# Kernel tuning notes

Measured on AMD Instinct MI355X. Metric: run time of the kernel, lower is better.

## Reference

```python
import jax, jax.numpy as jnp
import numpy as np

D = 1024
H = 16
HD = D // H
FF = 4 * D
LN_EPS = 1e-5


def _layernorm(x, g, b):
    mu = jnp.mean(x, axis=-1, keepdims=True)
    var = jnp.mean(jnp.square(x - mu), axis=-1, keepdims=True)
    return (x - mu) / jnp.sqrt(var + LN_EPS) * g + b


def setup_inputs() -> dict:
    key = jax.random.key(0)
    ks = jax.random.split(key, 17)
    s = 0.02
    inp = {
        "x": jax.random.normal(ks[0], (2, 2048, D), dtype=jnp.float32),
        "Wq": jax.random.normal(ks[1], (D, D), dtype=jnp.float32) * s,
        "bq": jnp.zeros((D,), jnp.float32),
        "Wk": jax.random.normal(ks[2], (D, D), dtype=jnp.float32) * s,
        "bk": jnp.zeros((D,), jnp.float32),
        "Wv": jax.random.normal(ks[3], (D, D), dtype=jnp.float32) * s,
        "bv": jnp.zeros((D,), jnp.float32),
        "Wo": jax.random.normal(ks[4], (D, D), dtype=jnp.float32) * s,
        "bo": jnp.zeros((D,), jnp.float32),
        "ln1_g": jnp.ones((D,), jnp.float32),
        "ln1_b": jnp.zeros((D,), jnp.float32),
        "W1": jax.random.normal(ks[5], (D, FF), dtype=jnp.float32) * s,
        "b1": jnp.zeros((FF,), jnp.float32),
        "W2": jax.random.normal(ks[6], (FF, D), dtype=jnp.float32) * s,
        "b2": jnp.zeros((D,), jnp.float32),
        "ln2_g": jnp.ones((D,), jnp.float32),
        "ln2_b": jnp.zeros((D,), jnp.float32),
    }
    return inp


def reference(x, Wq, bq, Wk, bk, Wv, bv, Wo, bo, ln1_g, ln1_b, W1, b1, W2, b2, ln2_g, ln2_b):
    bs, seq, _ = x.shape
    # qkv projections -> [b, h, s, hd]
    def split_heads(t):
        return t.reshape(bs, seq, H, HD).transpose(0, 2, 1, 3)
    q = split_heads(x @ Wq + bq)
    k = split_heads(x @ Wk + bk)
    v = split_heads(x @ Wv + bv)
    # causal attention (explicit, matching source math)
    scores = jnp.einsum('bhqd,bhkd->bhqk', q, k) / jnp.sqrt(jnp.float32(HD))
    causal = jnp.tril(jnp.ones((seq, seq), dtype=bool))
    scores = jnp.where(causal, scores, -jnp.inf)
    attn = jax.nn.softmax(scores, axis=-1)
    ctx = jnp.einsum('bhqk,bhkd->bhqd', attn, v)
    ctx = ctx.transpose(0, 2, 1, 3).reshape(bs, seq, D)
    attn_out = ctx @ Wo + bo
    # residual + LN1
    h = _layernorm(attn_out + x, ln1_g, ln1_b)
    # GELU MLP (exact erf gelu, torch nn.GELU default)
    ffn = jax.nn.gelu(h @ W1 + b1, approximate=False) @ W2 + b2
    # residual + LN2
    out = _layernorm(ffn + h, ln2_g, ln2_b)
    return out
```

## Files before the change

### kernel.cpp

```cpp
#include <hip/hip_runtime.h>

#define D_MODEL 1024
#define SEQ 2048
#define NHEAD 16
#define HDIM 64
#define FF_DIM 4096
#define NTOK 4096

using bf16x8 = __attribute__((ext_vector_type(8))) short;
using f32x4  = __attribute__((ext_vector_type(4))) float;
typedef unsigned short ushort_t;

__device__ __forceinline__ unsigned short f2bu(float f) {
    unsigned int u = __float_as_uint(f);
    unsigned int r = u + 0x7FFFu + ((u >> 16) & 1u);
    return (unsigned short)(r >> 16);
}
__device__ __forceinline__ float b2f(unsigned short u) {
    union { unsigned int i; float f; } x;
    x.i = ((unsigned int)u) << 16;
    return x.f;
}

typedef __attribute__((address_space(1))) const unsigned int* gas_ptr;
typedef __attribute__((address_space(3))) unsigned int* las_ptr;
__device__ __forceinline__ void gload_lds16(const void* g, void* l) {
    __builtin_amdgcn_global_load_lds((gas_ptr)g, (las_ptr)l, 16, 0, 0);
}

__device__ __forceinline__ float gelu_f(float x) {
    float z = 1.59576912f * x * (1.f + 0.044715f * x * x);
    float t = __expf(z);
    float th = (t - 1.f) / (t + 1.f);
    return 0.5f * x * (1.f + th);
}

__global__ void cast_f32_to_bf16(const float* __restrict__ in, ushort_t* __restrict__ out, int n8) {
    int i = blockIdx.x * blockDim.x + threadIdx.x;
    if (i >= n8) return;
    const float4* p = (const float4*)in + (size_t)i * 2;
    float4 a = p[0], b = p[1];
    uint4 o;
    o.x = (unsigned)f2bu(a.x) | ((unsigned)f2bu(a.y) << 16);
    o.y = (unsigned)f2bu(a.z) | ((unsigned)f2bu(a.w) << 16);
    o.z = (unsigned)f2bu(b.x) | ((unsigned)f2bu(b.y) << 16);
    o.w = (unsigned)f2bu(b.z) | ((unsigned)f2bu(b.w) << 16);
    ((uint4*)out)[i] = o;
}

__global__ void transpose_f32_to_bf16(const float* __restrict__ in, ushort_t* __restrict__ out, int R, int C) {
    __shared__ float tile[64][65];
    int bx = blockIdx.x * 64, by = blockIdx.y * 64;
    int tx = threadIdx.x & 63, ty = threadIdx.x >> 6;
#pragma unroll
    for (int i = 0; i < 64; i += 4)
        tile[ty + i][tx] = in[(size_t)(by + ty + i) * C + bx + tx];
    __syncthreads();
#pragma unroll
    for (int i = 0; i < 64; i += 4)
        out[(size_t)(bx + ty + i) * R + by + tx] = f2bu(tile[tx][ty + i]);
}

__global__ __launch_bounds__(256)
void gemm_bf16(const ushort_t* __restrict__ A, const ushort_t* __restrict__ Bt,
               const float* __restrict__ bias, int bias_per_row,
               ushort_t* __restrict__ outb, float* __restrict__ outf,
               int M, int N, int K, float out_scale, int do_gelu) {
    __shared__ char lds[2 * 128 * 128];
    char* Al = lds;
    char* Bl = lds + 128 * 128;
    const int tid = threadIdx.x;
    const int l = tid & 63, w = tid >> 6;
    const int wr = w >> 1, wc = w & 1;
    const int g = l >> 4, l15 = l & 15;
    const int m0 = blockIdx.x * 128, n0 = blockIdx.y * 128;

    f32x4 acc[4][4] = {};
    const int nk = K >> 6;
    const int srow = l >> 3;
    const int scol = (l & 7) * 8;
    const ushort_t* Ab = A + (size_t)(m0 + w * 32 + srow) * K + scol;
    const ushort_t* Bb = Bt + (size_t)(n0 + w * 32 + srow) * K + scol;

    for (int kt = 0; kt < nk; ++kt) {
        __syncthreads();
        const size_t ko = (size_t)kt * 64;
#pragma unroll
        for (int c = 0; c < 4; ++c) {
            gload_lds16(Ab + (size_t)c * 8 * K + ko, Al + (w * 4 + c) * 1024);
            gload_lds16(Bb + (size_t)c * 8 * K + ko, Bl + (w * 4 + c) * 1024);
        }
        __syncthreads();
#pragma unroll
        for (int ks = 0; ks < 2; ks++) {
            bf16x8 af[4];
#pragma unroll
            for (int m = 0; m < 4; m++)
                af[m] = *(const bf16x8*)(Al + (wr * 64 + m * 16 + l15) * 128 + (ks * 4 + g) * 16);
#pragma unroll
            for (int n = 0; n < 4; n++) {
                bf16x8 bfr = *(const bf16x8*)(Bl + (wc * 64 + n * 16 + l15) * 128 + (ks * 4 + g) * 16);
#pragma unroll
                for (int m = 0; m < 4; m++)
                    acc[m][n] = __builtin_amdgcn_mfma_f32_16x16x32_bf16(af[m], bfr, acc[m][n], 0, 0, 0);
            }
        }
    }
#pragma unroll
    for (int m = 0; m < 4; m++) {
        int row0 = m0 + wr * 64 + m * 16 + g * 4;
#pragma unroll
        for (int n = 0; n < 4; n++) {
            int col = n0 + wc * 64 + n * 16 + l15;
            float bc = bias_per_row ? 0.f : bias[col];
#pragma unroll
            for (int jj = 0; jj < 4; jj++) {
                int row = row0 + jj;
                float v = acc[m][n][jj] + (bias_per_row ? bias[row] : bc);
                v *= out_scale;
                if (do_gelu) v = gelu_f(v);
                size_t idx = (size_t)row * N + col;
                if (outb) outb[idx] = f2bu(v);
                else      outf[idx] = v;
            }
        }
    }
}

__global__ __launch_bounds__(256)
void attn_fwd(const ushort_t* __restrict__ qg, const ushort_t* __restrict__ kg,
              const ushort_t* __restrict__ vtg, ushort_t* __restrict__ ctx) {
    __shared__ char plds[4 * 16 * 144];
    const int tid = threadIdx.x;
    const int l = tid & 63, w = tid >> 6;
    const int g = l >> 4, l15 = l & 15;
    const int bid = blockIdx.x;
    const int xcd = bid & 7;
    const int slot = bid >> 3;
    const int QBi = slot & 31;
    const int grp = slot >> 5;
    const int h = xcd + 8 * (grp & 1);
    const int b = grp >> 1;
    const int q0 = QBi * 64;
    const int qrow = b * SEQ + q0 + w * 16 + l15;
    const int q_local = w * 16 + l15;

    const ushort_t* qp = qg + (size_t)qrow * D_MODEL + h * HDIM + g * 8;
    bf16x8 qf0 = *(const bf16x8*)qp;
    bf16x8 qf1 = *(const bf16x8*)(qp + 32);

    const ushort_t* kbase = kg + ((size_t)(b * SEQ + l15) * D_MODEL) + h * HDIM + g * 8;
    const ushort_t* vbase = vtg + (size_t)(h * HDIM + l15) * NTOK + b * SEQ + g * 8;

    f32x4 O[4] = {};
    float m_run = -1e30f, l_run = 0.f;
    char* pl = plds + w * (16 * 144) + l15 * 144;

    bf16x8 kf[8];
    bf16x8 vf[8];
#pragma unroll
    for (int md = 0; md < 4; ++md) {
        const ushort_t* kp = kbase + (size_t)(md * 16) * D_MODEL;
        kf[2 * md]     = *(const bf16x8*)kp;
        kf[2 * md + 1] = *(const bf16x8*)(kp + 32);
    }

    for (int t = 0; t <= QBi; ++t) {
        const int kv0 = t * 64;
#pragma unroll
        for (int md = 0; md < 4; ++md) {
            const ushort_t* vp = vbase + (size_t)(md * 16) * NTOK + kv0;
            vf[2 * md]     = *(const bf16x8*)vp;
            vf[2 * md + 1] = *(const bf16x8*)(vp + 32);
        }
        f32x4 s[4];
#pragma unroll
        for (int md = 0; md < 4; ++md) {
            f32x4 z = {0.f, 0.f, 0.f, 0.f};
            z = __builtin_amdgcn_mfma_f32_16x16x32_bf16(kf[2 * md], qf0, z, 0, 0, 0);
            z = __builtin_amdgcn_mfma_f32_16x16x32_bf16(kf[2 * md + 1], qf1, z, 0, 0, 0);
            s[md] = z;
        }
        {
            const int tn = (t < QBi) ? (t + 1) : t;
#pragma unroll
            for (int md = 0; md < 4; ++md) {
                const ushort_t* kp = kbase + (size_t)(tn * 64 + md * 16) * D_MODEL;
                kf[2 * md]     = *(const bf16x8*)kp;
                kf[2 * md + 1] = *(const bf16x8*)(kp + 32);
            }
        }
        if (t == QBi) {
#pragma unroll
            for (int md = 0; md < 4; ++md)
#pragma unroll
                for (int jj = 0; jj < 4; jj++) {
                    int kvl = md * 16 + g * 4 + jj;
                    if (kvl > q_local) s[md][jj] = -1e30f;
                }
        }
        float pmax = -1e30f;
#pragma unroll
        for (int md = 0; md < 4; ++md)
#pragma unroll
            for (int jj = 0; jj < 4; jj++) pmax = fmaxf(pmax, s[md][jj]);
        pmax = fmaxf(pmax, __shfl_xor(pmax, 16));
        pmax = fmaxf(pmax, __shfl_xor(pmax, 32));
        float mnew = fmaxf(m_run, pmax);
        float sc = __expf(m_run - mnew);
        float rsum = 0.f;
#pragma unroll
        for (int md = 0; md < 4; ++md) {
            float p0 = __expf(s[md][0] - mnew);
            float p1 = __expf(s[md][1] - mnew);
            float p2 = __expf(s[md][2] - mnew);
            float p3 = __expf(s[md][3] - mnew);
            rsum += (p0 + p1) + (p2 + p3);
            uint2 pk;
            pk.x = (unsigned)f2bu(p0) | ((unsigned)f2bu(p1) << 16);
            pk.y = (unsigned)f2bu(p2) | ((unsigned)f2bu(p3) << 16);
            *(uint2*)(pl + (md * 16 + g * 4) * 2) = pk;
        }
        rsum += __shfl_xor(rsum, 16);
        rsum += __shfl_xor(rsum, 32);
        l_run = l_run * sc + rsum;
        m_run = mnew;
#pragma unroll
        for (int md = 0; md < 4; ++md) {
            O[md][0] *= sc; O[md][1] *= sc; O[md][2] *= sc; O[md][3] *= sc;
        }
#pragma unroll
        for (int ks = 0; ks < 2; ++ks) {
            bf16x8 pf = *(const bf16x8*)(pl + ks * 64 + g * 16);
#pragma unroll
            for (int md = 0; md < 4; ++md)
                O[md] = __builtin_amdgcn_mfma_f32_16x16x32_bf16(vf[2 * md + ks], pf, O[md], 0, 0, 0);
        }
    }
    float rl = 1.f / l_run;
#pragma unroll
    for (int md = 0; md < 4; ++md) {
        uint2 o;
        o.x = (unsigned)f2bu(O[md][0] * rl) | ((unsigned)f2bu(O[md][1] * rl) << 16);
        o.y = (unsigned)f2bu(O[md][2] * rl) | ((unsigned)f2bu(O[md][3] * rl) << 16);
        *(uint2*)(ctx + (size_t)qrow * D_MODEL + h * HDIM + md * 16 + g * 4) = o;
    }
}

__global__ __launch_bounds__(256)
void ln_kernel(const ushort_t* __restrict__ a, const ushort_t* __restrict__ resb,
               const float* __restrict__ resf,
               const float* __restrict__ gam, const float* __restrict__ bet,
               ushort_t* __restrict__ outb, float* __restrict__ outf) {
    const int w = threadIdx.x >> 6, l = threadIdx.x & 63;
    const int row = blockIdx.x * 4 + w;
    const size_t base = (size_t)row * D_MODEL + l * 16;
    float r[16];
    int4 av0 = *(const int4*)(a + base);
    int4 av1 = *(const int4*)(a + base + 8);
    const unsigned short* u0 = (const unsigned short*)&av0;
    const unsigned short* u1 = (const unsigned short*)&av1;
#pragma unroll
    for (int i = 0; i < 8; i++) { r[i] = b2f(u0[i]); r[8 + i] = b2f(u1[i]); }
    if (resf) {
        const float4* rp = (const float4*)(resf + base);
#pragma unroll
        for (int i = 0; i < 4; i++) {
            float4 f = rp[i];
            r[i * 4 + 0] += f.x; r[i * 4 + 1] += f.y; r[i * 4 + 2] += f.z; r[i * 4 + 3] += f.w;
        }
    } else {
        int4 rv0 = *(const int4*)(resb + base);
        int4 rv1 = *(const int4*)(resb + base + 8);
        const unsigned short* v0 = (const unsigned short*)&rv0;
        const unsigned short* v1 = (const unsigned short*)&rv1;
#pragma unroll
        for (int i = 0; i < 8; i++) { r[i] += b2f(v0[i]); r[8 + i] += b2f(v1[i]); }
    }
    float s = 0.f;
#pragma unroll
    for (int i = 0; i < 16; i++) s += r[i];
#pragma unroll
    for (int m = 1; m < 64; m <<= 1) s += __shfl_xor(s, m);
    float mu = s * (1.f / 1024.f);
    float v = 0.f;
#pragma unroll
    for (int i = 0; i < 16; i++) { float d = r[i] - mu; v += d * d; }
#pragma unroll
    for (int m = 1; m < 64; m <<= 1) v += __shfl_xor(v, m);
    float rstd = rsqrtf(v * (1.f / 1024.f) + 1e-5f);
    float o[16];
    const float4* gp = (const float4*)(gam + l * 16);
    const float4* bp = (const float4*)(bet + l * 16);
#pragma unroll
    for (int i = 0; i < 4; i++) {
        float4 gv = gp[i], bv = bp[i];
        o[i * 4 + 0] = (r[i * 4 + 0] - mu) * rstd * gv.x + bv.x;
        o[i * 4 + 1] = (r[i * 4 + 1] - mu) * rstd * gv.y + bv.y;
        o[i * 4 + 2] = (r[i * 4 + 2] - mu) * rstd * gv.z + bv.z;
        o[i * 4 + 3] = (r[i * 4 + 3] - mu) * rstd * gv.w + bv.w;
    }
    if (outb) {
        uint4 w0, w1;
        unsigned* pw0 = (unsigned*)&w0;
        unsigned* pw1 = (unsigned*)&w1;
#pragma unroll
        for (int i = 0; i < 4; i++) {
            pw0[i] = (unsigned)f2bu(o[i * 2]) | ((unsigned)f2bu(o[i * 2 + 1]) << 16);
            pw1[i] = (unsigned)f2bu(o[8 + i * 2]) | ((unsigned)f2bu(o[8 + i * 2 + 1]) << 16);
        }
        *(uint4*)(outb + base) = w0;
        *(uint4*)(outb + base + 8) = w1;
    } else {
        float4* op = (float4*)(outf + base);
#pragma unroll
        for (int i = 0; i < 4; i++)
            op[i] = make_float4(o[i * 4], o[i * 4 + 1], o[i * 4 + 2], o[i * 4 + 3]);
    }
}

extern "C" void kernel_launch(void* const* d_in, const int* in_sizes, int n_in,
                              void* d_out, int out_size, void* d_ws, size_t ws_size,
                              hipStream_t stream) {
    const float* x     = (const float*)d_in[0];
    const float* Wq    = (const float*)d_in[1];
    const float* bq    = (const float*)d_in[2];
    const float* Wk    = (const float*)d_in[3];
    const float* bk    = (const float*)d_in[4];
    const float* Wv    = (const float*)d_in[5];
    const float* bv    = (const float*)d_in[6];
    const float* Wo    = (const float*)d_in[7];
    const float* bo    = (const float*)d_in[8];
    const float* ln1_g = (const float*)d_in[9];
    const float* ln1_b = (const float*)d_in[10];
    const float* W1    = (const float*)d_in[11];
    const float* b1    = (const float*)d_in[12];
    const float* W2    = (const float*)d_in[13];
    const float* b2    = (const float*)d_in[14];
    const float* ln2_g = (const float*)d_in[15];
    const float* ln2_b = (const float*)d_in[16];
    float* out = (float*)d_out;

    char* ws = (char*)d_ws;
    const size_t SZ = (size_t)NTOK * D_MODEL * 2;
    ushort_t* xb  = (ushort_t*)(ws + 0 * SZ);
    ushort_t* qb  = (ushort_t*)(ws + 1 * SZ);
    ushort_t* kb  = (ushort_t*)(ws + 2 * SZ);
    ushort_t* vt  = (ushort_t*)(ws + 3 * SZ);
    ushort_t* ctx = (ushort_t*)(ws + 4 * SZ);
    ushort_t* aob = (ushort_t*)(ws + 5 * SZ);
    ushort_t* hb  = (ushort_t*)(ws + 6 * SZ);
    char* wts = ws + 7 * SZ;
    ushort_t* wqt = (ushort_t*)(wts + 0x000000);
    ushort_t* wkt = (ushort_t*)(wts + 0x200000);
    ushort_t* wvt = (ushort_t*)(wts + 0x400000);
    ushort_t* wot = (ushort_t*)(wts + 0x600000);
    ushort_t* w1t = (ushort_t*)(wts + 0x800000);
    ushort_t* w2t = (ushort_t*)(wts + 0x1000000);
    ushort_t* f1b = (ushort_t*)(ws + 0 * SZ);
    ushort_t* f2b = (ushort_t*)(ws + 4 * SZ);
    if (ws_size < (size_t)(7 * SZ) + 0x1800000) return;

    cast_f32_to_bf16<<<2048, 256, 0, stream>>>(x, xb, NTOK * D_MODEL / 8);
    transpose_f32_to_bf16<<<dim3(16, 16), 256, 0, stream>>>(Wq, wqt, 1024, 1024);
    transpose_f32_to_bf16<<<dim3(16, 16), 256, 0, stream>>>(Wk, wkt, 1024, 1024);
    transpose_f32_to_bf16<<<dim3(16, 16), 256, 0, stream>>>(Wv, wvt, 1024, 1024);
    transpose_f32_to_bf16<<<dim3(16, 16), 256, 0, stream>>>(Wo, wot, 1024, 1024);
    transpose_f32_to_bf16<<<dim3(64, 16), 256, 0, stream>>>(W1, w1t, 1024, 4096);
    transpose_f32_to_bf16<<<dim3(16, 64), 256, 0, stream>>>(W2, w2t, 4096, 1024);

    gemm_bf16<<<dim3(32, 8), 256, 0, stream>>>(xb, wqt, bq, 0, qb, nullptr, 4096, 1024, 1024, 0.125f, 0);
    gemm_bf16<<<dim3(32, 8), 256, 0, stream>>>(xb, wkt, bk, 0, kb, nullptr, 4096, 1024, 1024, 1.f, 0);
    gemm_bf16<<<dim3(8, 32), 256, 0, stream>>>(wvt, xb, bv, 1, vt, nullptr, 1024, 4096, 1024, 1.f, 0);

    attn_fwd<<<1024, 256, 0, stream>>>(qb, kb, vt, ctx);

    gemm_bf16<<<dim3(32, 8), 256, 0, stream>>>(ctx, wot, bo, 0, aob, nullptr, 4096, 1024, 1024, 1.f, 0);
    ln_kernel<<<1024, 256, 0, stream>>>(aob, nullptr, x, ln1_g, ln1_b, hb, nullptr);
    gemm_bf16<<<dim3(32, 32), 256, 0, stream>>>(hb, w1t, b1, 0, f1b, nullptr, 4096, 4096, 1024, 1.f, 1);
    gemm_bf16<<<dim3(32, 8), 256, 0, stream>>>(f1b, w2t, b2, 0, f2b, nullptr, 4096, 1024, 4096, 1.f, 0);
    ln_kernel<<<1024, 256, 0, stream>>>(f2b, hb, nullptr, ln2_g, ln2_b, nullptr, out);
}
```

Before: 593.0 us.

## Pair causal query blocks per attention CTA and use narrower GEMM tiles for N=1024

Each attention block now handles two query tiles, p and 31-p, so every CTA does roughly equal causal work, and the grid is halved to 512. The GEMM becomes a template on tile width BN, and the N=1024 projections and W2 use 128x64 tiles to double the CTA count and fill more CUs. Smaller tiles lower data reuse per CTA and add extra loads of the A operand, and the paired attention runs its two tiles one after the other within a block.

```diff
diff --git a/kernel.cpp b/kernel.cpp
--- a/kernel.cpp
+++ b/kernel.cpp
@@ -61,35 +61,39 @@
         out[(size_t)(bx + ty + i) * R + by + tx] = f2bu(tile[tx][ty + i]);
 }
 
+template<int BN>
 __global__ __launch_bounds__(256)
 void gemm_bf16(const ushort_t* __restrict__ A, const ushort_t* __restrict__ Bt,
                const float* __restrict__ bias, int bias_per_row,
                ushort_t* __restrict__ outb, float* __restrict__ outf,
                int M, int N, int K, float out_scale, int do_gelu) {
-    __shared__ char lds[2 * 128 * 128];
+    constexpr int NB  = BN / 32;
+    constexpr int BCH = BN / 32;
+    __shared__ char lds[(128 + BN) * 128];
     char* Al = lds;
     char* Bl = lds + 128 * 128;
     const int tid = threadIdx.x;
     const int l = tid & 63, w = tid >> 6;
     const int wr = w >> 1, wc = w & 1;
     const int g = l >> 4, l15 = l & 15;
-    const int m0 = blockIdx.x * 128, n0 = blockIdx.y * 128;
-
-    f32x4 acc[4][4] = {};
+    const int m0 = blockIdx.x * 128, n0 = blockIdx.y * BN;
+
+    f32x4 acc[4][NB] = {};
     const int nk = K >> 6;
     const int srow = l >> 3;
     const int scol = (l & 7) * 8;
     const ushort_t* Ab = A + (size_t)(m0 + w * 32 + srow) * K + scol;
-    const ushort_t* Bb = Bt + (size_t)(n0 + w * 32 + srow) * K + scol;
+    const ushort_t* Bb = Bt + (size_t)(n0 + w * (BN / 4) + srow) * K + scol;
 
     for (int kt = 0; kt < nk; ++kt) {
         __syncthreads();
         const size_t ko = (size_t)kt * 64;
 #pragma unroll
-        for (int c = 0; c < 4; ++c) {
+        for (int c = 0; c < 4; ++c)
             gload_lds16(Ab + (size_t)c * 8 * K + ko, Al + (w * 4 + c) * 1024);
-            gload_lds16(Bb + (size_t)c * 8 * K + ko, Bl + (w * 4 + c) * 1024);
-        }
+#pragma unroll
+        for (int c = 0; c < BCH; ++c)
+            gload_lds16(Bb + (size_t)c * 8 * K + ko, Bl + (w * BCH + c) * 1024);
         __syncthreads();
 #pragma unroll
         for (int ks = 0; ks < 2; ks++) {
@@ -98,8 +102,8 @@
             for (int m = 0; m < 4; m++)
                 af[m] = *(const bf16x8*)(Al + (wr * 64 + m * 16 + l15) * 128 + (ks * 4 + g) * 16);
 #pragma unroll
-            for (int n = 0; n < 4; n++) {
-                bf16x8 bfr = *(const bf16x8*)(Bl + (wc * 64 + n * 16 + l15) * 128 + (ks * 4 + g) * 16);
+            for (int n = 0; n < NB; n++) {
+                bf16x8 bfr = *(const bf16x8*)(Bl + (wc * (BN / 2) + n * 16 + l15) * 128 + (ks * 4 + g) * 16);
 #pragma unroll
                 for (int m = 0; m < 4; m++)
                     acc[m][n] = __builtin_amdgcn_mfma_f32_16x16x32_bf16(af[m], bfr, acc[m][n], 0, 0, 0);
@@ -110,8 +114,8 @@
     for (int m = 0; m < 4; m++) {
         int row0 = m0 + wr * 64 + m * 16 + g * 4;
 #pragma unroll
-        for (int n = 0; n < 4; n++) {
-            int col = n0 + wc * 64 + n * 16 + l15;
+        for (int n = 0; n < NB; n++) {
+            int col = n0 + wc * (BN / 2) + n * 16 + l15;
             float bc = bias_per_row ? 0.f : bias[col];
 #pragma unroll
             for (int jj = 0; jj < 4; jj++) {
@@ -137,113 +141,118 @@
     const int bid = blockIdx.x;
     const int xcd = bid & 7;
     const int slot = bid >> 3;
-    const int QBi = slot & 31;
-    const int grp = slot >> 5;
+    const int p = slot & 15;
+    const int grp = slot >> 4;
     const int h = xcd + 8 * (grp & 1);
     const int b = grp >> 1;
-    const int q0 = QBi * 64;
-    const int qrow = b * SEQ + q0 + w * 16 + l15;
     const int q_local = w * 16 + l15;
-
-    const ushort_t* qp = qg + (size_t)qrow * D_MODEL + h * HDIM + g * 8;
-    bf16x8 qf0 = *(const bf16x8*)qp;
-    bf16x8 qf1 = *(const bf16x8*)(qp + 32);
 
     const ushort_t* kbase = kg + ((size_t)(b * SEQ + l15) * D_MODEL) + h * HDIM + g * 8;
     const ushort_t* vbase = vtg + (size_t)(h * HDIM + l15) * NTOK + b * SEQ + g * 8;
-
-    f32x4 O[4] = {};
-    float m_run = -1e30f, l_run = 0.f;
     char* pl = plds + w * (16 * 144) + l15 * 144;
 
     bf16x8 kf[8];
     bf16x8 vf[8];
-#pragma unroll
-    for (int md = 0; md < 4; ++md) {
-        const ushort_t* kp = kbase + (size_t)(md * 16) * D_MODEL;
-        kf[2 * md]     = *(const bf16x8*)kp;
-        kf[2 * md + 1] = *(const bf16x8*)(kp + 32);
-    }
-
-    for (int t = 0; t <= QBi; ++t) {
-        const int kv0 = t * 64;
+
+#pragma unroll
+    for (int phase = 0; phase < 2; ++phase) {
+        const int QBi = phase ? (31 - p) : p;
+        const int qrow = b * SEQ + QBi * 64 + w * 16 + l15;
+
+        const ushort_t* qp = qg + (size_t)qrow * D_MODEL + h * HDIM + g * 8;
+        bf16x8 qf0 = *(const bf16x8*)qp;
+        bf16x8 qf1 = *(const bf16x8*)(qp + 32);
+
+        f32x4 O[4] = {};
+        float m_run = -1e30f, l_run = 0.f;
+
 #pragma unroll
         for (int md = 0; md < 4; ++md) {
-            const ushort_t* vp = vbase + (size_t)(md * 16) * NTOK + kv0;
-            vf[2 * md]     = *(const bf16x8*)vp;
-            vf[2 * md + 1] = *(const bf16x8*)(vp + 32);
-        }
-        f32x4 s[4];
+            const ushort_t* kp = kbase + (size_t)(md * 16) * D_MODEL;
+            kf[2 * md]     = *(const bf16x8*)kp;
+            kf[2 * md + 1] = *(const bf16x8*)(kp + 32);
+        }
+
+        for (int t = 0; t <= QBi; ++t) {
+            const int kv0 = t * 64;
+#pragma unroll
+            for (int md = 0; md < 4; ++md) {
+                const ushort_t* vp = vbase + (size_t)(md * 16) * NTOK + kv0;
+                vf[2 * md]     = *(const bf16x8*)vp;
+                vf[2 * md + 1] = *(const bf16x8*)(vp + 32);
+            }
+            f32x4 s[4];
+#pragma unroll
+            for (int md = 0; md < 4; ++md) {
+                f32x4 z = {0.f, 0.f, 0.f, 0.f};
+                z = __builtin_amdgcn_mfma_f32_16x16x32_bf16(kf[2 * md], qf0, z, 0, 0, 0);
+                z = __builtin_amdgcn_mfma_f32_16x16x32_bf16(kf[2 * md + 1], qf1, z, 0, 0, 0);
+                s[md] = z;
+            }
+            {
+                const int tn = (t < QBi) ? (t + 1) : t;
+#pragma unroll
+                for (int md = 0; md < 4; ++md) {
+                    const ushort_t* kp = kbase + (size_t)(tn * 64 + md * 16) * D_MODEL;
+                    kf[2 * md]     = *(const bf16x8*)kp;
+                    kf[2 * md + 1] = *(const bf16x8*)(kp + 32);
+                }
+            }
+            if (t == QBi) {
+#pragma unroll
+                for (int md = 0; md < 4; ++md)
+#pragma unroll
+                    for (int jj = 0; jj < 4; jj++) {
+                        int kvl = md * 16 + g * 4 + jj;
+                        if (kvl > q_local) s[md][jj] = -1e30f;
+                    }
+            }
+            float pmax = -1e30f;
+#pragma unroll
+            for (int md = 0; md < 4; ++md)
+#pragma unroll
+                for (int jj = 0; jj < 4; jj++) pmax = fmaxf(pmax, s[md][jj]);
+            pmax = fmaxf(pmax, __shfl_xor(pmax, 16));
+            pmax = fmaxf(pmax, __shfl_xor(pmax, 32));
+            float mnew = fmaxf(m_run, pmax);
+            float sc = __expf(m_run - mnew);
+            float rsum = 0.f;
+#pragma unroll
+            for (int md = 0; md < 4; ++md) {
+                float p0 = __expf(s[md][0] - mnew);
+                float p1 = __expf(s[md][1] - mnew);
+                float p2 = __expf(s[md][2] - mnew);
+                float p3 = __expf(s[md][3] - mnew);
+                rsum += (p0 + p1) + (p2 + p3);
+                uint2 pk;
+                pk.x = (unsigned)f2bu(p0) | ((unsigned)f2bu(p1) << 16);
+                pk.y = (unsigned)f2bu(p2) | ((unsigned)f2bu(p3) << 16);
+                *(uint2*)(pl + (md * 16 + g * 4) * 2) = pk;
+            }
+            rsum += __shfl_xor(rsum, 16);
+            rsum += __shfl_xor(rsum, 32);
+            l_run = l_run * sc + rsum;
+            m_run = mnew;
+#pragma unroll
+            for (int md = 0; md < 4; ++md) {
+                O[md][0] *= sc; O[md][1] *= sc; O[md][2] *= sc; O[md][3] *= sc;
+            }
+#pragma unroll
+            for (int ks = 0; ks < 2; ++ks) {
+                bf16x8 pf = *(const bf16x8*)(pl + ks * 64 + g * 16);
+#pragma unroll
+                for (int md = 0; md < 4; ++md)
+                    O[md] = __builtin_amdgcn_mfma_f32_16x16x32_bf16(vf[2 * md + ks], pf, O[md], 0, 0, 0);
+            }
+        }
+        float rl = 1.f / l_run;
 #pragma unroll
         for (int md = 0; md < 4; ++md) {
-            f32x4 z = {0.f, 0.f, 0.f, 0.f};
-            z = __builtin_amdgcn_mfma_f32_16x16x32_bf16(kf[2 * md], qf0, z, 0, 0, 0);
-            z = __builtin_amdgcn_mfma_f32_16x16x32_bf16(kf[2 * md + 1], qf1, z, 0, 0, 0);
-            s[md] = z;
-        }
-        {
-            const int tn = (t < QBi) ? (t + 1) : t;
-#pragma unroll
-            for (int md = 0; md < 4; ++md) {
-                const ushort_t* kp = kbase + (size_t)(tn * 64 + md * 16) * D_MODEL;
-                kf[2 * md]     = *(const bf16x8*)kp;
-                kf[2 * md + 1] = *(const bf16x8*)(kp + 32);
-            }
-        }
-        if (t == QBi) {
-#pragma unroll
-            for (int md = 0; md < 4; ++md)
-#pragma unroll
-                for (int jj = 0; jj < 4; jj++) {
-                    int kvl = md * 16 + g * 4 + jj;
-                    if (kvl > q_local) s[md][jj] = -1e30f;
-                }
-        }
-        float pmax = -1e30f;
-#pragma unroll
-        for (int md = 0; md < 4; ++md)
-#pragma unroll
-            for (int jj = 0; jj < 4; jj++) pmax = fmaxf(pmax, s[md][jj]);
-        pmax = fmaxf(pmax, __shfl_xor(pmax, 16));
-        pmax = fmaxf(pmax, __shfl_xor(pmax, 32));
-        float mnew = fmaxf(m_run, pmax);
-        float sc = __expf(m_run - mnew);
-        float rsum = 0.f;
-#pragma unroll
-        for (int md = 0; md < 4; ++md) {
-            float p0 = __expf(s[md][0] - mnew);
-            float p1 = __expf(s[md][1] - mnew);
-            float p2 = __expf(s[md][2] - mnew);
-            float p3 = __expf(s[md][3] - mnew);
-            rsum += (p0 + p1) + (p2 + p3);
-            uint2 pk;
-            pk.x = (unsigned)f2bu(p0) | ((unsigned)f2bu(p1) << 16);
-            pk.y = (unsigned)f2bu(p2) | ((unsigned)f2bu(p3) << 16);
-            *(uint2*)(pl + (md * 16 + g * 4) * 2) = pk;
-        }
-        rsum += __shfl_xor(rsum, 16);
-        rsum += __shfl_xor(rsum, 32);
-        l_run = l_run * sc + rsum;
-        m_run = mnew;
-#pragma unroll
-        for (int md = 0; md < 4; ++md) {
-            O[md][0] *= sc; O[md][1] *= sc; O[md][2] *= sc; O[md][3] *= sc;
-        }
-#pragma unroll
-        for (int ks = 0; ks < 2; ++ks) {
-            bf16x8 pf = *(const bf16x8*)(pl + ks * 64 + g * 16);
-#pragma unroll
-            for (int md = 0; md < 4; ++md)
-                O[md] = __builtin_amdgcn_mfma_f32_16x16x32_bf16(vf[2 * md + ks], pf, O[md], 0, 0, 0);
-        }
-    }
-    float rl = 1.f / l_run;
-#pragma unroll
-    for (int md = 0; md < 4; ++md) {
-        uint2 o;
-        o.x = (unsigned)f2bu(O[md][0] * rl) | ((unsigned)f2bu(O[md][1] * rl) << 16);
-        o.y = (unsigned)f2bu(O[md][2] * rl) | ((unsigned)f2bu(O[md][3] * rl) << 16);
-        *(uint2*)(ctx + (size_t)qrow * D_MODEL + h * HDIM + md * 16 + g * 4) = o;
+            uint2 o;
+            o.x = (unsigned)f2bu(O[md][0] * rl) | ((unsigned)f2bu(O[md][1] * rl) << 16);
+            o.y = (unsigned)f2bu(O[md][2] * rl) | ((unsigned)f2bu(O[md][3] * rl) << 16);
+            *(uint2*)(ctx + (size_t)qrow * D_MODEL + h * HDIM + md * 16 + g * 4) = o;
+        }
     }
 }
 
@@ -369,15 +378,15 @@
     transpose_f32_to_bf16<<<dim3(64, 16), 256, 0, stream>>>(W1, w1t, 1024, 4096);
     transpose_f32_to_bf16<<<dim3(16, 64), 256, 0, stream>>>(W2, w2t, 4096, 1024);
 
-    gemm_bf16<<<dim3(32, 8), 256, 0, stream>>>(xb, wqt, bq, 0, qb, nullptr, 4096, 1024, 1024, 0.125f, 0);
-    gemm_bf16<<<dim3(32, 8), 256, 0, stream>>>(xb, wkt, bk, 0, kb, nullptr, 4096, 1024, 1024, 1.f, 0);
-    gemm_bf16<<<dim3(8, 32), 256, 0, stream>>>(wvt, xb, bv, 1, vt, nullptr, 1024, 4096, 1024, 1.f, 0);
-
-    attn_fwd<<<1024, 256, 0, stream>>>(qb, kb, vt, ctx);
-
-    gemm_bf16<<<dim3(32, 8), 256, 0, stream>>>(ctx, wot, bo, 0, aob, nullptr, 4096, 1024, 1024, 1.f, 0);
+    gemm_bf16<64><<<dim3(32, 16), 256, 0, stream>>>(xb, wqt, bq, 0, qb, nullptr, 4096, 1024, 1024, 0.125f, 0);
+    gemm_bf16<64><<<dim3(32, 16), 256, 0, stream>>>(xb, wkt, bk, 0, kb, nullptr, 4096, 1024, 1024, 1.f, 0);
+    gemm_bf16<64><<<dim3(8, 64), 256, 0, stream>>>(wvt, xb, bv, 1, vt, nullptr, 1024, 4096, 1024, 1.f, 0);
+
+    attn_fwd<<<512, 256, 0, stream>>>(qb, kb, vt, ctx);
+
+    gemm_bf16<64><<<dim3(32, 16), 256, 0, stream>>>(ctx, wot, bo, 0, aob, nullptr, 4096, 1024, 1024, 1.f, 0);
     ln_kernel<<<1024, 256, 0, stream>>>(aob, nullptr, x, ln1_g, ln1_b, hb, nullptr);
-    gemm_bf16<<<dim3(32, 32), 256, 0, stream>>>(hb, w1t, b1, 0, f1b, nullptr, 4096, 4096, 1024, 1.f, 1);
-    gemm_bf16<<<dim3(32, 8), 256, 0, stream>>>(f1b, w2t, b2, 0, f2b, nullptr, 4096, 1024, 4096, 1.f, 0);
+    gemm_bf16<128><<<dim3(32, 32), 256, 0, stream>>>(hb, w1t, b1, 0, f1b, nullptr, 4096, 4096, 1024, 1.f, 1);
+    gemm_bf16<64><<<dim3(32, 16), 256, 0, stream>>>(f1b, w2t, b2, 0, f2b, nullptr, 4096, 1024, 4096, 1.f, 0);
     ln_kernel<<<1024, 256, 0, stream>>>(f2b, hb, nullptr, ln2_g, ln2_b, nullptr, out);
 }
```

Measured after the change: 524.5 us. 11.5% less time.
